# Performance work log

Measured on AMD Instinct MI355X. Metric: run time of the kernel, lower is better.

## Reference

```python
import jax, jax.numpy as jnp
import numpy as np

V, E, H, L = 50257, 256, 1024, 2   # vocab, embed_dim, hidden_dim, num_layers
B, T, K = 64, 80, 5                # batch, max_len, top_k
TEMP = 0.75
TWO_PI_OVER_24 = np.float32(2.0 * np.pi / 24.0)


def setup_inputs() -> dict:
    key = jax.random.key(0)
    ks = jax.random.split(key, 12)
    n = lambda i, shape, s: (jax.random.normal(ks[i], shape, jnp.float32) * s)
    hours = jax.random.uniform(ks[0], (B,), jnp.float32) * 24.0
    return {
        "hours": hours,
        "tp_w1": n(1, (2, H), 0.5),
        "tp_b1": jnp.zeros((H,), jnp.float32),
        "tp_w2": n(2, (H, 2 * L * H), 0.02),
        "tp_b2": jnp.zeros((2 * L * H,), jnp.float32),
        "embed": n(3, (V, E), 0.1).at[0].set(0.0),  # padding_idx=0 row zeroed
        "w_ih0": n(4, (E, 4 * H), 0.05),
        "w_hh0": n(5, (H, 4 * H), 0.05),
        "b0": jnp.zeros((4 * H,), jnp.float32),     # b_ih + b_hh combined
        "w_ih1": n(6, (H, 4 * H), 0.05),
        "w_hh1": n(7, (H, 4 * H), 0.05),
        "b1": jnp.zeros((4 * H,), jnp.float32),
        "fc_w": n(8, (H, V), 0.02),
        "fc_b": jnp.zeros((V,), jnp.float32),
        "sos_id": 1,
    }


def _lstm_cell(x, h, c, w_ih, w_hh, b):
    # torch gate order: i, f, g, o
    g = x @ w_ih + h @ w_hh + b
    i, f, gg, o = jnp.split(g, 4, axis=-1)
    c2 = jax.nn.sigmoid(f) * c + jax.nn.sigmoid(i) * jnp.tanh(gg)
    h2 = jax.nn.sigmoid(o) * jnp.tanh(c2)
    return h2, c2


def reference(hours, tp_w1, tp_b1, tp_w2, tp_b2, embed,
              w_ih0, w_hh0, b0, w_ih1, w_hh1, b1, fc_w, fc_b, sos_id):
    # _encode_time: sin/cos of hour angle -> MLP -> (h0, c0) per layer
    a = hours * TWO_PI_OVER_24
    feat = jnp.stack([jnp.sin(a), jnp.cos(a)], axis=-1)          # [B,2]
    tp = jnp.tanh(feat @ tp_w1 + tp_b1) @ tp_w2 + tp_b2          # [B,2*L*H]
    tp = tp.reshape(B, L, 2, H)
    h = jnp.transpose(tp[:, :, 0, :], (1, 0, 2))                 # [L,B,H]
    c = jnp.transpose(tp[:, :, 1, :], (1, 0, 2))                 # [L,B,H]

    keys = jax.random.split(jax.random.key(42), T)

    def step(carry, k):
        h, c, tok = carry
        x = embed[tok]                                           # [B,E]
        h0n, c0n = _lstm_cell(x, h[0], c[0], w_ih0, w_hh0, b0)
        h1n, c1n = _lstm_cell(h0n, h[1], c[1], w_ih1, w_hh1, b1)
        logits = (h1n @ fc_w + fc_b) / TEMP                      # [B,V]
        topv, topi = jax.lax.top_k(logits, K)                    # [B,K]
        probs = jax.nn.softmax(topv, axis=-1)
        sel = jax.random.categorical(k, topv, axis=-1)           # [B], == multinomial(probs)
        nxt = jnp.take_along_axis(topi, sel[:, None], axis=1)[:, 0]
        return (jnp.stack([h0n, h1n]), jnp.stack([c0n, c1n]), nxt), (nxt, probs)

    tok0 = jnp.full((B,), sos_id, jnp.int32)
    _, (toks, probs) = jax.lax.scan(step, (h, c, tok0), keys)
    # toks: [T,B] -> [B,T]; probs: [T,B,K] -> [B,T,K]
    return jnp.transpose(toks, (1, 0)), jnp.transpose(probs, (1, 0, 2))
```

## Files before the change

### kernel.cpp

```cpp
#include <hip/hip_runtime.h>
#include <math.h>
#include <stdint.h>
#include <limits.h>

#define VSZ 50257
#define ESZ 256
#define HSZ 1024
#define BSZ 64
#define TSZ 80
#define GC  4096
#define NFCB 786
#define NCAND (NFCB*5)
#define NSLOT 13
#define NREF 16

typedef unsigned int u32;
typedef unsigned short u16;
typedef double f64x4 __attribute__((ext_vector_type(4)));
typedef float f32x4v __attribute__((ext_vector_type(4)));
typedef __bf16 bf16x8 __attribute__((ext_vector_type(8)));
union BFrag { u16 u[8]; bf16x8 v; };

__device__ __forceinline__ u16 f2bf(float f) {
  u32 x = __float_as_uint(f);
  return (u16)((x + 0x7FFFu + ((x >> 16) & 1u)) >> 16);
}
__device__ __forceinline__ float bf2f(u16 h) { return __uint_as_float(((u32)h) << 16); }

__device__ __forceinline__ void tf2x32(u32 k0, u32 k1, u32& x0, u32& x1) {
  u32 ks2 = k0 ^ k1 ^ 0x1BD11BDAu;
  x0 += k0; x1 += k1;
#define RND(r) { x0 += x1; x1 = (x1 << r) | (x1 >> (32 - r)); x1 ^= x0; }
  RND(13) RND(15) RND(26) RND(6)
  x0 += k1; x1 += ks2 + 1u;
  RND(17) RND(29) RND(16) RND(24)
  x0 += ks2; x1 += k0 + 2u;
  RND(13) RND(15) RND(26) RND(6)
  x0 += k0; x1 += k1 + 3u;
  RND(17) RND(29) RND(16) RND(24)
  x0 += k1; x1 += ks2 + 4u;
  RND(13) RND(15) RND(26) RND(6)
  x0 += ks2; x1 += k0 + 5u;
#undef RND
}

__device__ __forceinline__ double dsig(double x) { return 0.5 + 0.5 * tanh(0.5 * x); }

__device__ __forceinline__ void ins5(double v, int i, double* tv, int* ti) {
  bool beat4 = (v > tv[4]) || (v == tv[4] && i < ti[4]);
  if (!beat4) return;
  tv[4] = v; ti[4] = i;
#pragma unroll
  for (int p = 4; p > 0; --p) {
    bool sw = (tv[p] > tv[p-1]) || (tv[p] == tv[p-1] && ti[p] < ti[p-1]);
    double a0 = sw ? tv[p] : tv[p-1]; double a1 = sw ? tv[p-1] : tv[p];
    tv[p-1] = a0; tv[p] = a1;
    int b0 = sw ? ti[p] : ti[p-1]; int b1 = sw ? ti[p-1] : ti[p];
    ti[p-1] = b0; ti[p] = b1;
  }
}

__device__ __forceinline__ double dref(int m, int n) {
  int s = 0;
#pragma unroll
  for (int k = 0; k < 4; ++k) s += (4*m + k + 1) * (16*k + n + 1);
  return (double)s;
}

__global__ __launch_bounds__(64) void k_probe(int* __restrict__ fbp) {
  int l = threadIdx.x;
  int lane16 = l & 15, sub = l >> 4;
  {
    double av = (double)(4 * lane16 + sub + 1);
    double bv = (double)(16 * sub + lane16 + 1);
    f64x4 acc = {0., 0., 0., 0.};
    acc = __builtin_amdgcn_mfma_f64_16x16x4f64(av, bv, acc, 0, 0, 0);
    bool o0 = true, o1 = true, o2 = true, o3 = true;
#pragma unroll
    for (int j = 0; j < 4; ++j) {
      double d = acc[j];
      o0 = o0 && (d == dref(4 * sub + j, lane16));
      o1 = o1 && (d == dref(lane16, 4 * sub + j));
      o2 = o2 && (d == dref(sub + 4 * j, lane16));
      o3 = o3 && (d == dref(lane16, sub + 4 * j));
    }
    int a0 = __all(o0), a1 = __all(o1), a2 = __all(o2), a3 = __all(o3);
    if (l == 0) { fbp[0] = a0 ? 0 : a1 ? 1 : a2 ? 2 : 3; fbp[1] = 0; }
  }
  {
    BFrag fa, fbv;
#pragma unroll
    for (int i = 0; i < 8; ++i) {
      int k = sub * 8 + i;
      fa.u[i]  = f2bf((float)((lane16 * 5 + k * 3) % 63 + 1));
      fbv.u[i] = f2bf((float)((k * 7 + lane16 * 11) % 61 + 1));
    }
    f32x4v c = {0.f, 0.f, 0.f, 0.f};
    c = __builtin_amdgcn_mfma_f32_16x16x32_bf16(fa.v, fbv.v, c, 0, 0, 0);
    bool okb = true;
#pragma unroll
    for (int j = 0; j < 4; ++j) {
      int mm = sub * 4 + j, nn = lane16;
      int ref = 0;
      for (int k = 0; k < 32; ++k) ref += ((mm*5 + k*3) % 63 + 1) * ((k*7 + nn*11) % 61 + 1);
      okb = okb && (c[j] == (float)ref);
    }
    int allb = __all(okb);
    if (l == 0) fbp[2] = allb;
  }
}

__global__ __launch_bounds__(256) void k_wconv(const float* __restrict__ W, u16* __restrict__ whT) {
  __shared__ u16 tile[64][65];
  int vb = blockIdx.x * 64, kb = blockIdx.y * 64;
  int tid = threadIdx.x;
#pragma unroll
  for (int i = 0; i < 16; ++i) {
    int r = i * 4 + (tid >> 6), c = tid & 63;
    int v = vb + c;
    tile[c][r] = (v < VSZ) ? f2bf(W[(size_t)(kb + r) * VSZ + v]) : (u16)0;
  }
  __syncthreads();
#pragma unroll
  for (int i = 0; i < 16; ++i) {
    int r = i * 4 + (tid >> 6), c = tid & 63;
    int v = vb + r;
    if (v < VSZ) whT[(size_t)v * 1024 + kb + c] = tile[r][c];
  }
}

__global__ __launch_bounds__(256) void k_rng(double* __restrict__ gum) {
  int idx = blockIdx.x * 256 + threadIdx.x;
  if (idx >= TSZ * 320) return;
  int t = idx / 320, m = idx % 320;
  u32 a0 = 0u, a1 = (u32)t;
  tf2x32(0u, 42u, a0, a1);
  u32 x0 = 0u, x1 = (u32)m;
  tf2x32(a0, a1, x0, x1);
  u32 bits = x0 ^ x1;
  const float TINY = 1.17549435082228750797e-38f;
  float f = __uint_as_float((bits >> 9) | 0x3f800000u) - 1.0f;
  float u = f + TINY;
  u = fmaxf(TINY, u);
  gum[idx] = -log(-log((double)u));
}

__global__ __launch_bounds__(256) void k_time1(const float* __restrict__ hours, const float* __restrict__ w1,
                                               const float* __restrict__ bb1, double* __restrict__ tp1T) {
  int idx = blockIdx.x * 256 + threadIdx.x;
  int b = idx & 63, hcol = idx >> 6;
  const float TPO = (float)(2.0 * 3.14159265358979323846 / 24.0);
  float af = hours[b] * TPO;
  double a = (double)af;
  double sv = sin(a), cv = cos(a);
  double vv = tanh(sv * (double)w1[hcol] + cv * (double)w1[HSZ + hcol] + (double)bb1[hcol]);
  tp1T[(size_t)hcol * 64 + b] = vv;
}

__global__ __launch_bounds__(256) void k_gemm_simple(const double* __restrict__ XTa, const float* __restrict__ Wa,
                                                     int Ka, int Sa, double* __restrict__ part) {
  int j = blockIdx.x * 256 + threadIdx.x;
  if (j >= GC) return;
  int s = blockIdx.y;
  int kc = Ka / Sa, k0 = s * kc;
  double acc[BSZ];
#pragma unroll
  for (int b = 0; b < BSZ; ++b) acc[b] = 0.0;
  const float* wp = Wa + (size_t)k0 * GC + j;
  const double* xp = XTa + (size_t)k0 * 64;
  for (int k = 0; k < kc; ++k) {
    double wv = (double)wp[0]; wp += GC;
#pragma unroll
    for (int b = 0; b < BSZ; ++b) acc[b] = fma(wv, xp[b], acc[b]);
    xp += 64;
  }
  double* o = part + ((size_t)s * 64) * GC + j;
#pragma unroll
  for (int b = 0; b < BSZ; ++b) o[(size_t)b * GC] = acc[b];
}

__global__ __launch_bounds__(256) void k_t2r(const double* __restrict__ part, const float* __restrict__ b2,
                                             double* __restrict__ h0T, double* __restrict__ c0,
                                             double* __restrict__ h1T, double* __restrict__ c1) {
  int b = blockIdx.y;
  int j = blockIdx.x * 256 + threadIdx.x;
  double acc = (double)b2[j];
  for (int s = 0; s < 8; ++s) acc += part[((size_t)s * 64 + b) * GC + j];
  int l = j >> 11, half = (j >> 10) & 1, hcol = j & 1023;
  if (half == 0) (l ? h1T : h0T)[(size_t)hcol * 64 + b] = acc;
  else           (l ? c1 : c0)[(size_t)b * HSZ + hcol] = acc;
}

__global__ __launch_bounds__(256, 4) void k_lstm_mfma(const double* __restrict__ x0, const float* __restrict__ W0,
                                                      const double* __restrict__ x1, const float* __restrict__ W1,
                                                      const double* __restrict__ x2, const float* __restrict__ W2,
                                                      int s1, int s2, double* __restrict__ part,
                                                      const int* __restrict__ fbp) {
  int conv = fbp[0] & 3;
  __shared__ double xs[64 * 64];
  int tid = threadIdx.x;
  int l = tid & 63, wv = tid >> 6;
  int sub = l >> 4, lane16 = l & 15;
  int colbase = blockIdx.x * 64;
  int s = blockIdx.y;
  const double* XT; const float* W; int k0;
  if (s < s1)      { XT = x0; W = W0; k0 = s * 256; }
  else if (s < s2) { XT = x1; W = W1; k0 = (s - s1) * 256; }
  else             { XT = x2; W = W2; k0 = (s - s2) * 256; }
  int colA = colbase + wv * 16 + lane16;
  f64x4 a0 = {0.,0.,0.,0.}, a1 = {0.,0.,0.,0.}, a2 = {0.,0.,0.,0.}, a3 = {0.,0.,0.,0.};
  const float* wp = W + (size_t)(k0 + sub) * GC + colA;
  float ab[8];
#pragma unroll
  for (int u = 0; u < 8; ++u) { ab[u] = wp[0]; wp += (size_t)4 * GC; }
  for (int ch = 0; ch < 4; ++ch) {
    __syncthreads();
    const double2* src = (const double2*)(XT + (size_t)(k0 + ch * 64) * 64);
    double2* dst = (double2*)xs;
    for (int i = tid; i < 2048; i += 256) dst[i] = src[i];
    __syncthreads();
#pragma unroll
    for (int g = 0; g < 2; ++g) {
#pragma unroll
      for (int u = 0; u < 8; ++u) {
        int ks = g * 8 + u;
        int step = ch * 16 + ks;
        float nv = 0.f;
        if (step + 8 < 64) nv = wp[0];
        wp += (size_t)4 * GC;
        double av = (double)ab[u];
        const double* bp = xs + (ks * 4 + sub) * 64 + lane16;
        double b0 = bp[0], b1 = bp[16], b2 = bp[32], b3 = bp[48];
        a0 = __builtin_amdgcn_mfma_f64_16x16x4f64(av, b0, a0, 0, 0, 0);
        a1 = __builtin_amdgcn_mfma_f64_16x16x4f64(av, b1, a1, 0, 0, 0);
        a2 = __builtin_amdgcn_mfma_f64_16x16x4f64(av, b2, a2, 0, 0, 0);
        a3 = __builtin_amdgcn_mfma_f64_16x16x4f64(av, b3, a3, 0, 0, 0);
        ab[u] = nv;
      }
    }
  }
#pragma unroll
  for (int j = 0; j < 4; ++j) {
    int m = (conv == 0) ? sub * 4 + j : (conv == 2) ? sub + 4 * j : lane16;
    int n = (conv == 0) ? lane16 : (conv == 2) ? lane16 : ((conv == 1) ? sub * 4 + j : sub + 4 * j);
    size_t base = ((size_t)s * 64 + n) * GC + colbase + wv * 16 + m;
    part[base]                   = a0[j];
    part[base + (size_t)16 * GC] = a1[j];
    part[base + (size_t)32 * GC] = a2[j];
    part[base + (size_t)48 * GC] = a3[j];
  }
}

__global__ __launch_bounds__(256) void k_cell(const double* __restrict__ part, int sBeg, int S,
                                              const float* __restrict__ bias,
                                              double* __restrict__ c, double* __restrict__ hT,
                                              int emit, u16* __restrict__ xh) {
  int b = blockIdx.y;
  int hcol = blockIdx.x * 256 + threadIdx.x;
  double gi = (double)bias[hcol];
  double gf = (double)bias[1024 + hcol];
  double gg = (double)bias[2048 + hcol];
  double go = (double)bias[3072 + hcol];
#pragma unroll 4
  for (int s = sBeg; s < sBeg + S; ++s) {
    const double* p = part + ((size_t)s * 64 + b) * GC;
    gi += p[hcol]; gf += p[1024 + hcol]; gg += p[2048 + hcol]; go += p[3072 + hcol];
  }
  size_t ci = (size_t)b * HSZ + hcol;
  double cn = dsig(gf) * c[ci] + dsig(gi) * tanh(gg);
  double hn = dsig(go) * tanh(cn);
  c[ci] = cn;
  hT[(size_t)hcol * 64 + b] = hn;
  if (emit)
    xh[(size_t)(hcol >> 7) * 8192 + (size_t)b * 128 + (hcol & 127)] = f2bf((float)hn);
}

__global__ __launch_bounds__(256, 4) void k_fcbf(const u16* __restrict__ xhg, const u16* __restrict__ whT,
                                                 const float* __restrict__ fcb,
                                                 double* __restrict__ candV, int* __restrict__ candI,
                                                 const int* __restrict__ fbp) {
  if (fbp[2] == 0) return;
  __shared__ double xs[64 * 64];
  u16* lx = (u16*)xs;
  int tid = threadIdx.x;
  int l = tid & 63, wv = tid >> 6;
  int sub = l >> 4, lane16 = l & 15;
  int vbase = blockIdx.x * 64;
  int colA = min(vbase + wv * 16 + lane16, VSZ - 1);
  const u16* wrow = whT + (size_t)colA * 1024;
  f32x4v acc0 = {0,0,0,0}, acc1 = {0,0,0,0}, acc2 = {0,0,0,0}, acc3 = {0,0,0,0};
  for (int ch = 0; ch < 8; ++ch) {
    bf16x8 wh0 = *(const bf16x8*)(wrow + ch * 128 + 0 * 32 + sub * 8);
    bf16x8 wh1 = *(const bf16x8*)(wrow + ch * 128 + 1 * 32 + sub * 8);
    bf16x8 wh2 = *(const bf16x8*)(wrow + ch * 128 + 2 * 32 + sub * 8);
    bf16x8 wh3 = *(const bf16x8*)(wrow + ch * 128 + 3 * 32 + sub * 8);
    __syncthreads();
    {
      const uint4* sg = (const uint4*)(xhg + (size_t)ch * 8192);
      uint4* dl = (uint4*)lx;
#pragma unroll
      for (int i = 0; i < 4; ++i) {
        int u = tid + i * 256;
        int bswz = u >> 4, g = u & 15;
        dl[(bswz << 4) | (g ^ (bswz & 7))] = sg[u];
      }
    }
    __syncthreads();
#pragma unroll
    for (int kt = 0; kt < 4; ++kt) {
      bf16x8 whv = (kt == 0) ? wh0 : (kt == 1) ? wh1 : (kt == 2) ? wh2 : wh3;
#define BT_STEP(BT, ACC) {                                                              \
        int bb = BT * 16 + lane16;                                                      \
        const bf16x8* bp2 = (const bf16x8*)lx + ((bb << 4) | ((kt * 4 + sub) ^ (bb & 7))); \
        ACC = __builtin_amdgcn_mfma_f32_16x16x32_bf16(whv, *bp2, ACC, 0, 0, 0); }
      BT_STEP(0, acc0)
      BT_STEP(1, acc1)
      BT_STEP(2, acc2)
      BT_STEP(3, acc3)
#undef BT_STEP
    }
  }
  __syncthreads();
#pragma unroll
  for (int j = 0; j < 4; ++j) {
    int vl = wv * 16 + sub * 4 + j;
    int v = vbase + vl;
    bool okv = (v < VSZ);
    double bi = okv ? (double)fcb[min(v, VSZ - 1)] : 0.0;
    int b0i = lane16, b1i = 16 + lane16, b2i = 32 + lane16, b3i = 48 + lane16;
    xs[b0i * 64 + ((vl + b0i) & 63)] = okv ? ((double)acc0[j] + bi) / 0.75 : -INFINITY;
    xs[b1i * 64 + ((vl + b1i) & 63)] = okv ? ((double)acc1[j] + bi) / 0.75 : -INFINITY;
    xs[b2i * 64 + ((vl + b2i) & 63)] = okv ? ((double)acc2[j] + bi) / 0.75 : -INFINITY;
    xs[b3i * 64 + ((vl + b3i) & 63)] = okv ? ((double)acc3[j] + bi) / 0.75 : -INFINITY;
  }
  __syncthreads();
  if (tid < 64) {
    int b = tid;
    double tv[5]; int ti[5];
#pragma unroll
    for (int p = 0; p < 5; ++p) { tv[p] = -INFINITY; ti[p] = INT_MAX; }
    for (int vl2 = 0; vl2 < 64; ++vl2)
      ins5(xs[b * 64 + ((vl2 + b) & 63)], vbase + vl2, tv, ti);
#pragma unroll
    for (int r = 0; r < 5; ++r) {
      candV[(size_t)b * NCAND + blockIdx.x * 5 + r] = tv[r];
      candI[(size_t)b * NCAND + blockIdx.x * 5 + r] = ti[r];
    }
  }
}

__global__ __launch_bounds__(256, 4) void k_fcf64(const double* __restrict__ h1T, const float* __restrict__ W,
                                                  const float* __restrict__ fcb,
                                                  double* __restrict__ candV, int* __restrict__ candI,
                                                  const int* __restrict__ fbp) {
  int conv = fbp[0] & 3;
  __shared__ double xs[64 * 64];
  int tid = threadIdx.x;
  int l = tid & 63, wv = tid >> 6;
  int sub = l >> 4, lane16 = l & 15;
  int vbase = blockIdx.x * 64;
  int colA = min(vbase + wv * 16 + lane16, VSZ - 1);
  f64x4 a0 = {0.,0.,0.,0.}, a1 = {0.,0.,0.,0.}, a2 = {0.,0.,0.,0.}, a3 = {0.,0.,0.,0.};
  const float* wp = W + (size_t)sub * VSZ + colA;
  float ab[8];
#pragma unroll
  for (int u = 0; u < 8; ++u) { ab[u] = wp[0]; wp += (size_t)4 * VSZ; }
  for (int ch = 0; ch < 16; ++ch) {
    __syncthreads();
    const double2* src = (const double2*)(h1T + (size_t)ch * 64 * 64);
    double2* dst = (double2*)xs;
    for (int i = tid; i < 2048; i += 256) dst[i] = src[i];
    __syncthreads();
#pragma unroll
    for (int g = 0; g < 2; ++g) {
#pragma unroll
      for (int u = 0; u < 8; ++u) {
        int ks = g * 8 + u;
        int step = ch * 16 + ks;
        float nv = 0.f;
        if (step + 8 < 256) nv = wp[0];
        wp += (size_t)4 * VSZ;
        double av = (double)ab[u];
        const double* bp = xs + (ks * 4 + sub) * 64 + lane16;
        double b0 = bp[0], b1 = bp[16], b2 = bp[32], b3 = bp[48];
        a0 = __builtin_amdgcn_mfma_f64_16x16x4f64(av, b0, a0, 0, 0, 0);
        a1 = __builtin_amdgcn_mfma_f64_16x16x4f64(av, b1, a1, 0, 0, 0);
        a2 = __builtin_amdgcn_mfma_f64_16x16x4f64(av, b2, a2, 0, 0, 0);
        a3 = __builtin_amdgcn_mfma_f64_16x16x4f64(av, b3, a3, 0, 0, 0);
        ab[u] = nv;
      }
    }
  }
  __syncthreads();
#pragma unroll
  for (int j = 0; j < 4; ++j) {
    int m = (conv == 0) ? sub * 4 + j : (conv == 2) ? sub + 4 * j : lane16;
    int n = (conv == 0) ? lane16 : (conv == 2) ? lane16 : ((conv == 1) ? sub * 4 + j : sub + 4 * j);
    int vl = wv * 16 + m;
    int v = vbase + vl;
    bool okv = (v < VSZ);
    double bi = okv ? (double)fcb[min(v, VSZ - 1)] : 0.0;
    int b0i = n, b1i = 16 + n, b2i = 32 + n, b3i = 48 + n;
    xs[b0i * 64 + ((vl + b0i) & 63)] = okv ? (a0[j] + bi) / 0.75 : -INFINITY;
    xs[b1i * 64 + ((vl + b1i) & 63)] = okv ? (a1[j] + bi) / 0.75 : -INFINITY;
    xs[b2i * 64 + ((vl + b2i) & 63)] = okv ? (a2[j] + bi) / 0.75 : -INFINITY;
    xs[b3i * 64 + ((vl + b3i) & 63)] = okv ? (a3[j] + bi) / 0.75 : -INFINITY;
  }
  __syncthreads();
  if (tid < 64) {
    int b = tid;
    double tv[5]; int ti[5];
#pragma unroll
    for (int p = 0; p < 5; ++p) { tv[p] = -INFINITY; ti[p] = INT_MAX; }
    for (int vl2 = 0; vl2 < 64; ++vl2)
      ins5(xs[b * 64 + ((vl2 + b) & 63)], vbase + vl2, tv, ti);
#pragma unroll
    for (int r = 0; r < 5; ++r) {
      candV[(size_t)b * NCAND + blockIdx.x * 5 + r] = tv[r];
      candI[(size_t)b * NCAND + blockIdx.x * 5 + r] = ti[r];
    }
  }
}

__global__ __launch_bounds__(256) void k_rfin(const double* __restrict__ candV, const int* __restrict__ candI,
                                              const float* __restrict__ W, const float* __restrict__ fcb,
                                              const double* __restrict__ h1T,
                                              const double* __restrict__ gum, int t,
                                              const float* __restrict__ embed,
                                              float* __restrict__ out, double* __restrict__ xt0) {
  __shared__ float sv[NCAND];
  __shared__ int   si[NCAND];
  __shared__ double exS[NREF];
  __shared__ float wvv[4]; __shared__ int wvi[4]; __shared__ int wvs[4];
  int b = blockIdx.x, tid = threadIdx.x;
  int l = tid & 63, wvd = tid >> 6;
  for (int e = tid; e < NCAND; e += 256) {
    sv[e] = (float)candV[(size_t)b * NCAND + e];
    si[e] = candI[(size_t)b * NCAND + e];
  }
  __syncthreads();
  int cidx[NREF];
#pragma unroll
  for (int r = 0; r < NREF; ++r) {
    float bv = -INFINITY; int bi = INT_MAX, bs = 0;
    for (int e = tid; e < NCAND; e += 256) {
      float v = sv[e]; int i2 = si[e];
      if (v > bv || (v == bv && i2 < bi)) { bv = v; bi = i2; bs = e; }
    }
#pragma unroll
    for (int off = 1; off < 64; off <<= 1) {
      float ov = __shfl_xor(bv, off, 64);
      int oi = __shfl_xor(bi, off, 64);
      int os = __shfl_xor(bs, off, 64);
      if (ov > bv || (ov == bv && oi < bi)) { bv = ov; bi = oi; bs = os; }
    }
    if (l == 0) { wvv[wvd] = bv; wvi[wvd] = bi; wvs[wvd] = bs; }
    __syncthreads();
    float fv = wvv[0]; int fi = wvi[0], fs = wvs[0];
#pragma unroll
    for (int q = 1; q < 4; ++q) {
      float ov = wvv[q]; int oi = wvi[q], os = wvs[q];
      if (ov > fv || (ov == fv && oi < fi)) { fv = ov; fi = oi; fs = os; }
    }
    cidx[r] = fi;
    __syncthreads();
    if (tid == 0) sv[fs] = -INFINITY;
    __syncthreads();
  }
#pragma unroll
  for (int rr = 0; rr < 4; ++rr) {
    int c = wvd + rr * 4;
    int vc = cidx[c];
    double p = 0.0;
#pragma unroll
    for (int i = 0; i < 16; ++i) {
      int k = i * 64 + l;
      p = fma((double)W[(size_t)k * VSZ + vc], h1T[(size_t)k * 64 + b], p);
    }
#pragma unroll
    for (int off = 1; off < 64; off <<= 1) p += __shfl_xor(p, off, 64);
    if (l == 0) exS[c] = (p + (double)fcb[vc]) / 0.75;
  }
  __syncthreads();
  double tv[5]; int ti[5];
#pragma unroll
  for (int p = 0; p < 5; ++p) { tv[p] = -INFINITY; ti[p] = INT_MAX; }
#pragma unroll
  for (int c = 0; c < NREF; ++c) ins5(exS[c], cidx[c], tv, ti);
  const double* g = gum + (size_t)t * 320 + b * 5;
  double bestv = tv[0] + g[0]; int best = 0;
#pragma unroll
  for (int k2 = 1; k2 < 5; ++k2) { double vv2 = tv[k2] + g[k2]; if (vv2 > bestv) { bestv = vv2; best = k2; } }
  int nxt = ti[best];
  if (tid == 0) {
    out[b * TSZ + t] = (float)nxt;
    double m = tv[0];
    double exx[5]; double s = 0.0;
#pragma unroll
    for (int k2 = 0; k2 < 5; ++k2) { exx[k2] = exp(tv[k2] - m); s += exx[k2]; }
    float* po = out + BSZ * TSZ + ((size_t)b * TSZ + t) * 5;
#pragma unroll
    for (int k2 = 0; k2 < 5; ++k2) po[k2] = (float)(exx[k2] / s);
  }
  xt0[(size_t)tid * 64 + b] = (double)embed[(size_t)nxt * ESZ + tid];
}

__global__ __launch_bounds__(256) void k_emb0(const float* __restrict__ embed, const int* __restrict__ sos,
                                              double* __restrict__ xt0) {
  int idx = blockIdx.x * 256 + threadIdx.x;
  int b = idx & 63, k = idx >> 6;
  xt0[(size_t)k * 64 + b] = (double)embed[(size_t)sos[0] * ESZ + k];
}

extern "C" void kernel_launch(void* const* d_in, const int* in_sizes, int n_in,
                              void* d_out, int out_size, void* d_ws, size_t ws_size,
                              hipStream_t stream) {
  const float* hours = (const float*)d_in[0];
  const float* tp_w1 = (const float*)d_in[1];
  const float* tp_b1 = (const float*)d_in[2];
  const float* tp_w2 = (const float*)d_in[3];
  const float* tp_b2 = (const float*)d_in[4];
  const float* embed = (const float*)d_in[5];
  const float* w_ih0 = (const float*)d_in[6];
  const float* w_hh0 = (const float*)d_in[7];
  const float* b0    = (const float*)d_in[8];
  const float* w_ih1 = (const float*)d_in[9];
  const float* w_hh1 = (const float*)d_in[10];
  const float* b1    = (const float*)d_in[11];
  const float* fc_w  = (const float*)d_in[12];
  const float* fc_b  = (const float*)d_in[13];
  const int*   sos   = (const int*)d_in[14];
  float* out = (float*)d_out;

  char* w = (char*)d_ws;
  double* part = (double*)w;  w += (size_t)NSLOT * 64 * GC * 8;
  double* xt0  = (double*)w;  w += (size_t)ESZ * 64 * 8;
  double* h0T  = (double*)w;  w += (size_t)HSZ * 64 * 8;
  double* h1T  = (double*)w;  w += (size_t)HSZ * 64 * 8;
  double* c0   = (double*)w;  w += (size_t)BSZ * HSZ * 8;
  double* c1   = (double*)w;  w += (size_t)BSZ * HSZ * 8;
  double* tp1T = (double*)w;  w += (size_t)HSZ * 64 * 8;
  double* gum  = (double*)w;  w += (size_t)TSZ * 320 * 8;
  double* candV = (double*)w; w += (size_t)BSZ * NCAND * 8;
  int*    candI = (int*)w;    w += (size_t)BSZ * NCAND * 4;
  int*    fbuf  = (int*)w;    w += 64;
  u16*    xhg   = (u16*)w;    w += (size_t)HSZ * 64 * 2;
  u16*    whT   = (u16*)w;    w += (size_t)VSZ * 1024 * 2;
  size_t need = (size_t)(w - (char*)d_ws);
  int useBF = (ws_size >= need) ? 1 : 0;

  k_probe<<<dim3(1), dim3(64), 0, stream>>>(fbuf);
  k_rng<<<dim3(100), dim3(256), 0, stream>>>(gum);
  k_time1<<<dim3(256), dim3(256), 0, stream>>>(hours, tp_w1, tp_b1, tp1T);
  k_gemm_simple<<<dim3(16, 8), dim3(256), 0, stream>>>(tp1T, tp_w2, 1024, 8, part);
  k_t2r<<<dim3(16, 64), dim3(256), 0, stream>>>(part, tp_b2, h0T, c0, h1T, c1);
  k_emb0<<<dim3(64), dim3(256), 0, stream>>>(embed, sos, xt0);
  if (useBF)
    k_wconv<<<dim3(786, 16), dim3(256), 0, stream>>>(fc_w, whT);

  double* part9 = part + (size_t)9 * 64 * GC;
  for (int t = 0; t < TSZ; ++t) {
    k_lstm_mfma<<<dim3(64, 9), dim3(256), 0, stream>>>(xt0, w_ih0, h0T, w_hh0, h1T, w_hh1, 1, 5, part, fbuf);
    k_cell<<<dim3(4, 64), dim3(256), 0, stream>>>(part, 0, 5, b0, c0, h0T, 0, xhg);
    k_lstm_mfma<<<dim3(64, 4), dim3(256), 0, stream>>>(h0T, w_ih1, h0T, w_ih1, h0T, w_ih1, 4, 4, part9, fbuf);
    k_cell<<<dim3(4, 64), dim3(256), 0, stream>>>(part, 5, 8, b1, c1, h1T, 1, xhg);
    if (useBF)
      k_fcbf<<<dim3(NFCB), dim3(256), 0, stream>>>(xhg, whT, fc_b, candV, candI, fbuf);
    else
      k_fcf64<<<dim3(NFCB), dim3(256), 0, stream>>>(h1T, fc_w, fc_b, candV, candI, fbuf);
    k_rfin<<<dim3(64), dim3(256), 0, stream>>>(candV, candI, fc_w, fc_b, h1T, gum, t, embed, out, xt0);
  }
}
```

Before: 18.98 ms.

## Fuse per-timestep decode kernels into one persistent cooperative megakernel

```diff
diff --git a/kernel.cpp b/kernel.cpp
--- a/kernel.cpp
+++ b/kernel.cpp
@@ -1,4 +1,5 @@
 #include <hip/hip_runtime.h>
+#include <hip/hip_cooperative_groups.h>
 #include <math.h>
 #include <stdint.h>
 #include <limits.h>
@@ -13,6 +14,9 @@
 #define NCAND (NFCB*5)
 #define NSLOT 13
 #define NREF 16
+#define MGRID 576
+
+namespace cg = cooperative_groups;
 
 typedef unsigned int u32;
 typedef unsigned short u16;
@@ -191,22 +195,12 @@
   else           (l ? c1 : c0)[(size_t)b * HSZ + hcol] = acc;
 }
 
-__global__ __launch_bounds__(256, 4) void k_lstm_mfma(const double* __restrict__ x0, const float* __restrict__ W0,
-                                                      const double* __restrict__ x1, const float* __restrict__ W1,
-                                                      const double* __restrict__ x2, const float* __restrict__ W2,
-                                                      int s1, int s2, double* __restrict__ part,
-                                                      const int* __restrict__ fbp) {
-  int conv = fbp[0] & 3;
-  __shared__ double xs[64 * 64];
-  int tid = threadIdx.x;
+
+__device__ __forceinline__ void lstm_unit(int cb, int slot, const double* XT, const float* W, int k0,
+                                          double* part, int conv, double* xs, int tid) {
   int l = tid & 63, wv = tid >> 6;
   int sub = l >> 4, lane16 = l & 15;
-  int colbase = blockIdx.x * 64;
-  int s = blockIdx.y;
-  const double* XT; const float* W; int k0;
-  if (s < s1)      { XT = x0; W = W0; k0 = s * 256; }
-  else if (s < s2) { XT = x1; W = W1; k0 = (s - s1) * 256; }
-  else             { XT = x2; W = W2; k0 = (s - s2) * 256; }
+  int colbase = cb * 64;
   int colA = colbase + wv * 16 + lane16;
   f64x4 a0 = {0.,0.,0.,0.}, a1 = {0.,0.,0.,0.}, a2 = {0.,0.,0.,0.}, a3 = {0.,0.,0.,0.};
   const float* wp = W + (size_t)(k0 + sub) * GC + colA;
@@ -239,11 +233,12 @@
       }
     }
   }
+  __syncthreads();
 #pragma unroll
   for (int j = 0; j < 4; ++j) {
     int m = (conv == 0) ? sub * 4 + j : (conv == 2) ? sub + 4 * j : lane16;
     int n = (conv == 0) ? lane16 : (conv == 2) ? lane16 : ((conv == 1) ? sub * 4 + j : sub + 4 * j);
-    size_t base = ((size_t)s * 64 + n) * GC + colbase + wv * 16 + m;
+    size_t base = ((size_t)slot * 64 + n) * GC + colbase + wv * 16 + m;
     part[base]                   = a0[j];
     part[base + (size_t)16 * GC] = a1[j];
     part[base + (size_t)32 * GC] = a2[j];
@@ -251,12 +246,11 @@
   }
 }
 
-__global__ __launch_bounds__(256) void k_cell(const double* __restrict__ part, int sBeg, int S,
-                                              const float* __restrict__ bias,
-                                              double* __restrict__ c, double* __restrict__ hT,
-                                              int emit, u16* __restrict__ xh) {
-  int b = blockIdx.y;
-  int hcol = blockIdx.x * 256 + threadIdx.x;
+__device__ __forceinline__ void cell_unit(int u, const double* part, int sBeg, int S,
+                                          const float* bias, double* c, double* hT,
+                                          int emit, u16* xh, int tid) {
+  int b = u & 63;
+  int hcol = (u >> 6) * 256 + tid;
   double gi = (double)bias[hcol];
   double gf = (double)bias[1024 + hcol];
   double gg = (double)bias[2048 + hcol];
@@ -275,17 +269,12 @@
     xh[(size_t)(hcol >> 7) * 8192 + (size_t)b * 128 + (hcol & 127)] = f2bf((float)hn);
 }
 
-__global__ __launch_bounds__(256, 4) void k_fcbf(const u16* __restrict__ xhg, const u16* __restrict__ whT,
-                                                 const float* __restrict__ fcb,
-                                                 double* __restrict__ candV, int* __restrict__ candI,
-                                                 const int* __restrict__ fbp) {
-  if (fbp[2] == 0) return;
-  __shared__ double xs[64 * 64];
+__device__ __forceinline__ void fcbf_unit(int u, const u16* xhg, const u16* whT, const float* fcb,
+                                          double* candV, int* candI, double* xs, int tid) {
   u16* lx = (u16*)xs;
-  int tid = threadIdx.x;
   int l = tid & 63, wv = tid >> 6;
   int sub = l >> 4, lane16 = l & 15;
-  int vbase = blockIdx.x * 64;
+  int vbase = u * 64;
   int colA = min(vbase + wv * 16 + lane16, VSZ - 1);
   const u16* wrow = whT + (size_t)colA * 1024;
   f32x4v acc0 = {0,0,0,0}, acc1 = {0,0,0,0}, acc2 = {0,0,0,0}, acc3 = {0,0,0,0};
@@ -300,9 +289,9 @@
       uint4* dl = (uint4*)lx;
 #pragma unroll
       for (int i = 0; i < 4; ++i) {
-        int u = tid + i * 256;
-        int bswz = u >> 4, g = u & 15;
-        dl[(bswz << 4) | (g ^ (bswz & 7))] = sg[u];
+        int uu = tid + i * 256;
+        int bswz = uu >> 4, g = uu & 15;
+        dl[(bswz << 4) | (g ^ (bswz & 7))] = sg[uu];
       }
     }
     __syncthreads();
@@ -343,28 +332,24 @@
       ins5(xs[b * 64 + ((vl2 + b) & 63)], vbase + vl2, tv, ti);
 #pragma unroll
     for (int r = 0; r < 5; ++r) {
-      candV[(size_t)b * NCAND + blockIdx.x * 5 + r] = tv[r];
-      candI[(size_t)b * NCAND + blockIdx.x * 5 + r] = ti[r];
-    }
-  }
-}
-
-__global__ __launch_bounds__(256, 4) void k_fcf64(const double* __restrict__ h1T, const float* __restrict__ W,
-                                                  const float* __restrict__ fcb,
-                                                  double* __restrict__ candV, int* __restrict__ candI,
-                                                  const int* __restrict__ fbp) {
-  int conv = fbp[0] & 3;
-  __shared__ double xs[64 * 64];
-  int tid = threadIdx.x;
+      candV[(size_t)b * NCAND + u * 5 + r] = tv[r];
+      candI[(size_t)b * NCAND + u * 5 + r] = ti[r];
+    }
+  }
+  __syncthreads();
+}
+
+__device__ __forceinline__ void fcf64_unit(int u, const double* h1T, const float* W, const float* fcb,
+                                           double* candV, int* candI, int conv, double* xs, int tid) {
   int l = tid & 63, wv = tid >> 6;
   int sub = l >> 4, lane16 = l & 15;
-  int vbase = blockIdx.x * 64;
+  int vbase = u * 64;
   int colA = min(vbase + wv * 16 + lane16, VSZ - 1);
   f64x4 a0 = {0.,0.,0.,0.}, a1 = {0.,0.,0.,0.}, a2 = {0.,0.,0.,0.}, a3 = {0.,0.,0.,0.};
   const float* wp = W + (size_t)sub * VSZ + colA;
   float ab[8];
 #pragma unroll
-  for (int u = 0; u < 8; ++u) { ab[u] = wp[0]; wp += (size_t)4 * VSZ; }
+  for (int uu = 0; uu < 8; ++uu) { ab[uu] = wp[0]; wp += (size_t)4 * VSZ; }
   for (int ch = 0; ch < 16; ++ch) {
     __syncthreads();
     const double2* src = (const double2*)(h1T + (size_t)ch * 64 * 64);
@@ -374,20 +359,20 @@
 #pragma unroll
     for (int g = 0; g < 2; ++g) {
 #pragma unroll
-      for (int u = 0; u < 8; ++u) {
-        int ks = g * 8 + u;
+      for (int uu = 0; uu < 8; ++uu) {
+        int ks = g * 8 + uu;
         int step = ch * 16 + ks;
         float nv = 0.f;
         if (step + 8 < 256) nv = wp[0];
         wp += (size_t)4 * VSZ;
-        double av = (double)ab[u];
+        double av = (double)ab[uu];
         const double* bp = xs + (ks * 4 + sub) * 64 + lane16;
         double b0 = bp[0], b1 = bp[16], b2 = bp[32], b3 = bp[48];
         a0 = __builtin_amdgcn_mfma_f64_16x16x4f64(av, b0, a0, 0, 0, 0);
         a1 = __builtin_amdgcn_mfma_f64_16x16x4f64(av, b1, a1, 0, 0, 0);
         a2 = __builtin_amdgcn_mfma_f64_16x16x4f64(av, b2, a2, 0, 0, 0);
         a3 = __builtin_amdgcn_mfma_f64_16x16x4f64(av, b3, a3, 0, 0, 0);
-        ab[u] = nv;
+        ab[uu] = nv;
       }
     }
   }
@@ -416,10 +401,184 @@
       ins5(xs[b * 64 + ((vl2 + b) & 63)], vbase + vl2, tv, ti);
 #pragma unroll
     for (int r = 0; r < 5; ++r) {
-      candV[(size_t)b * NCAND + blockIdx.x * 5 + r] = tv[r];
-      candI[(size_t)b * NCAND + blockIdx.x * 5 + r] = ti[r];
-    }
-  }
+      candV[(size_t)b * NCAND + u * 5 + r] = tv[r];
+      candI[(size_t)b * NCAND + u * 5 + r] = ti[r];
+    }
+  }
+  __syncthreads();
+}
+
+__device__ __forceinline__ void rfin_unit(int b, const double* candV, const int* candI,
+                                          const float* W, const float* fcb, const double* h1T,
+                                          const double* gum, int t, const float* embed,
+                                          float* out, double* xt0, char* smem,
+                                          double* exS, float* wvv, int* wvi, int* wvs, int tid) {
+  float* sv = (float*)smem;
+  int*   si = (int*)(smem + NCAND * 4);
+  int l = tid & 63, wvd = tid >> 6;
+  for (int e = tid; e < NCAND; e += 256) {
+    sv[e] = (float)candV[(size_t)b * NCAND + e];
+    si[e] = candI[(size_t)b * NCAND + e];
+  }
+  __syncthreads();
+  int cidx[NREF];
+#pragma unroll
+  for (int r = 0; r < NREF; ++r) {
+    float bv = -INFINITY; int bi = INT_MAX, bs = 0;
+    for (int e = tid; e < NCAND; e += 256) {
+      float v = sv[e]; int i2 = si[e];
+      if (v > bv || (v == bv && i2 < bi)) { bv = v; bi = i2; bs = e; }
+    }
+#pragma unroll
+    for (int off = 1; off < 64; off <<= 1) {
+      float ov = __shfl_xor(bv, off, 64);
+      int oi = __shfl_xor(bi, off, 64);
+      int os = __shfl_xor(bs, off, 64);
+      if (ov > bv || (ov == bv && oi < bi)) { bv = ov; bi = oi; bs = os; }
+    }
+    if (l == 0) { wvv[wvd] = bv; wvi[wvd] = bi; wvs[wvd] = bs; }
+    __syncthreads();
+    float fv = wvv[0]; int fi = wvi[0], fs = wvs[0];
+#pragma unroll
+    for (int q = 1; q < 4; ++q) {
+      float ov = wvv[q]; int oi = wvi[q], os = wvs[q];
+      if (ov > fv || (ov == fv && oi < fi)) { fv = ov; fi = oi; fs = os; }
+    }
+    cidx[r] = fi;
+    __syncthreads();
+    if (tid == 0) sv[fs] = -INFINITY;
+    __syncthreads();
+  }
+#pragma unroll
+  for (int rr = 0; rr < 4; ++rr) {
+    int c = wvd + rr * 4;
+    int vc = cidx[c];
+    double p = 0.0;
+#pragma unroll
+    for (int i = 0; i < 16; ++i) {
+      int k = i * 64 + l;
+      p = fma((double)W[(size_t)k * VSZ + vc], h1T[(size_t)k * 64 + b], p);
+    }
+#pragma unroll
+    for (int off = 1; off < 64; off <<= 1) p += __shfl_xor(p, off, 64);
+    if (l == 0) exS[c] = (p + (double)fcb[vc]) / 0.75;
+  }
+  __syncthreads();
+  double tv[5]; int ti[5];
+#pragma unroll
+  for (int p = 0; p < 5; ++p) { tv[p] = -INFINITY; ti[p] = INT_MAX; }
+#pragma unroll
+  for (int c = 0; c < NREF; ++c) ins5(exS[c], cidx[c], tv, ti);
+  const double* g = gum + (size_t)t * 320 + b * 5;
+  double bestv = tv[0] + g[0]; int best = 0;
+#pragma unroll
+  for (int k2 = 1; k2 < 5; ++k2) { double vv2 = tv[k2] + g[k2]; if (vv2 > bestv) { bestv = vv2; best = k2; } }
+  int nxt = ti[best];
+  if (tid == 0) {
+    out[b * TSZ + t] = (float)nxt;
+    double m = tv[0];
+    double exx[5]; double s = 0.0;
+#pragma unroll
+    for (int k2 = 0; k2 < 5; ++k2) { exx[k2] = exp(tv[k2] - m); s += exx[k2]; }
+    float* po = out + BSZ * TSZ + ((size_t)b * TSZ + t) * 5;
+#pragma unroll
+    for (int k2 = 0; k2 < 5; ++k2) po[k2] = (float)(exx[k2] / s);
+  }
+  xt0[(size_t)tid * 64 + b] = (double)embed[(size_t)nxt * ESZ + tid];
+  __syncthreads();
+}
+
+struct MArgs {
+  double *xt0, *h0T, *h1T, *c0, *c1, *part, *gum, *candV;
+  int *candI, *fbuf;
+  u16 *xhg, *whT;
+  const float *w_ih0, *w_hh0, *b0, *w_ih1, *w_hh1, *b1, *fc_w, *fc_b, *embed;
+  float *out;
+  int useBF;
+};
+
+__global__ __launch_bounds__(256, 3) void k_mega(MArgs A) {
+  cg::grid_group grid = cg::this_grid();
+  __shared__ alignas(16) char smem[32768];
+  __shared__ double exS[NREF];
+  __shared__ float wvv[4]; __shared__ int wvi[4]; __shared__ int wvs[4];
+  double* xs = (double*)smem;
+  int tid = threadIdx.x;
+  int conv = A.fbuf[0] & 3;
+  int bf = A.useBF && (A.fbuf[2] != 0);
+  double* part9 = A.part + (size_t)9 * 64 * GC;
+  for (int t = 0; t < TSZ; ++t) {
+    for (int u = blockIdx.x; u < 576; u += gridDim.x) {
+      int cb = u & 63, s = u >> 6;
+      const double* XT; const float* W; int k0;
+      if (s < 1)      { XT = A.xt0; W = A.w_ih0; k0 = 0; }
+      else if (s < 5) { XT = A.h0T; W = A.w_hh0; k0 = (s - 1) * 256; }
+      else            { XT = A.h1T; W = A.w_hh1; k0 = (s - 5) * 256; }
+      lstm_unit(cb, s, XT, W, k0, A.part, conv, xs, tid);
+    }
+    grid.sync();
+    for (int u = blockIdx.x; u < 256; u += gridDim.x)
+      cell_unit(u, A.part, 0, 5, A.b0, A.c0, A.h0T, 0, A.xhg, tid);
+    grid.sync();
+    for (int u = blockIdx.x; u < 256; u += gridDim.x) {
+      int cb = u & 63, s = u >> 6;
+      lstm_unit(cb, 9 + s, A.h0T, A.w_ih1, s * 256, A.part, conv, xs, tid);
+    }
+    grid.sync();
+    for (int u = blockIdx.x; u < 256; u += gridDim.x)
+      cell_unit(u, A.part, 5, 8, A.b1, A.c1, A.h1T, 1, A.xhg, tid);
+    grid.sync();
+    if (bf) {
+      for (int u = blockIdx.x; u < NFCB; u += gridDim.x)
+        fcbf_unit(u, A.xhg, A.whT, A.fc_b, A.candV, A.candI, xs, tid);
+    } else {
+      for (int u = blockIdx.x; u < NFCB; u += gridDim.x)
+        fcf64_unit(u, A.h1T, A.fc_w, A.fc_b, A.candV, A.candI, conv, xs, tid);
+    }
+    grid.sync();
+    for (int u = blockIdx.x; u < 64; u += gridDim.x)
+      rfin_unit(u, A.candV, A.candI, A.fc_w, A.fc_b, A.h1T, A.gum, t, A.embed,
+                A.out, A.xt0, smem, exS, wvv, wvi, wvs, tid);
+    grid.sync();
+  }
+}
+
+
+__global__ __launch_bounds__(256, 4) void k_lstm_mfma(const double* __restrict__ x0, const float* __restrict__ W0,
+                                                      const double* __restrict__ x1, const float* __restrict__ W1,
+                                                      const double* __restrict__ x2, const float* __restrict__ W2,
+                                                      int s1, int s2, double* __restrict__ part,
+                                                      const int* __restrict__ fbp) {
+  __shared__ double xs[64 * 64];
+  int s = blockIdx.y;
+  const double* XT; const float* W; int k0;
+  if (s < s1)      { XT = x0; W = W0; k0 = s * 256; }
+  else if (s < s2) { XT = x1; W = W1; k0 = (s - s1) * 256; }
+  else             { XT = x2; W = W2; k0 = (s - s2) * 256; }
+  lstm_unit(blockIdx.x, s, XT, W, k0, part, fbp[0] & 3, xs, threadIdx.x);
+}
+
+__global__ __launch_bounds__(256) void k_cell(const double* __restrict__ part, int sBeg, int S,
+                                              const float* __restrict__ bias,
+                                              double* __restrict__ c, double* __restrict__ hT,
+                                              int emit, u16* __restrict__ xh) {
+  cell_unit(blockIdx.x * 64 + blockIdx.y, part, sBeg, S, bias, c, hT, emit, xh, threadIdx.x);
+}
+
+__global__ __launch_bounds__(256, 4) void k_fcbf(const u16* __restrict__ xhg, const u16* __restrict__ whT,
+                                                 const float* __restrict__ fcb,
+                                                 double* __restrict__ candV, int* __restrict__ candI,
+                                                 const int* __restrict__ fbp) {
+  __shared__ double xs[64 * 64];
+  fcbf_unit(blockIdx.x, xhg, whT, fcb, candV, candI, xs, threadIdx.x);
+}
+
+__global__ __launch_bounds__(256, 4) void k_fcf64(const double* __restrict__ h1T, const float* __restrict__ W,
+                                                  const float* __restrict__ fcb,
+                                                  double* __restrict__ candV, int* __restrict__ candI,
+                                                  const int* __restrict__ fbp) {
+  __shared__ double xs[64 * 64];
+  fcf64_unit(blockIdx.x, h1T, W, fcb, candV, candI, fbp[0] & 3, xs, threadIdx.x);
 }
 
 __global__ __launch_bounds__(256) void k_rfin(const double* __restrict__ candV, const int* __restrict__ candI,
@@ -428,81 +587,11 @@
                                               const double* __restrict__ gum, int t,
                                               const float* __restrict__ embed,
                                               float* __restrict__ out, double* __restrict__ xt0) {
-  __shared__ float sv[NCAND];
-  __shared__ int   si[NCAND];
+  __shared__ alignas(16) char smem[32768];
   __shared__ double exS[NREF];
   __shared__ float wvv[4]; __shared__ int wvi[4]; __shared__ int wvs[4];
-  int b = blockIdx.x, tid = threadIdx.x;
-  int l = tid & 63, wvd = tid >> 6;
-  for (int e = tid; e < NCAND; e += 256) {
-    sv[e] = (float)candV[(size_t)b * NCAND + e];
-    si[e] = candI[(size_t)b * NCAND + e];
-  }
-  __syncthreads();
-  int cidx[NREF];
-#pragma unroll
-  for (int r = 0; r < NREF; ++r) {
-    float bv = -INFINITY; int bi = INT_MAX, bs = 0;
-    for (int e = tid; e < NCAND; e += 256) {
-      float v = sv[e]; int i2 = si[e];
-      if (v > bv || (v == bv && i2 < bi)) { bv = v; bi = i2; bs = e; }
-    }
-#pragma unroll
-    for (int off = 1; off < 64; off <<= 1) {
-      float ov = __shfl_xor(bv, off, 64);
-      int oi = __shfl_xor(bi, off, 64);
-      int os = __shfl_xor(bs, off, 64);
-      if (ov > bv || (ov == bv && oi < bi)) { bv = ov; bi = oi; bs = os; }
-    }
-    if (l == 0) { wvv[wvd] = bv; wvi[wvd] = bi; wvs[wvd] = bs; }
-    __syncthreads();
-    float fv = wvv[0]; int fi = wvi[0], fs = wvs[0];
-#pragma unroll
-    for (int q = 1; q < 4; ++q) {
-      float ov = wvv[q]; int oi = wvi[q], os = wvs[q];
-      if (ov > fv || (ov == fv && oi < fi)) { fv = ov; fi = oi; fs = os; }
-    }
-    cidx[r] = fi;
-    __syncthreads();
-    if (tid == 0) sv[fs] = -INFINITY;
-    __syncthreads();
-  }
-#pragma unroll
-  for (int rr = 0; rr < 4; ++rr) {
-    int c = wvd + rr * 4;
-    int vc = cidx[c];
-    double p = 0.0;
-#pragma unroll
-    for (int i = 0; i < 16; ++i) {
-      int k = i * 64 + l;
-      p = fma((double)W[(size_t)k * VSZ + vc], h1T[(size_t)k * 64 + b], p);
-    }
-#pragma unroll
-    for (int off = 1; off < 64; off <<= 1) p += __shfl_xor(p, off, 64);
-    if (l == 0) exS[c] = (p + (double)fcb[vc]) / 0.75;
-  }
-  __syncthreads();
-  double tv[5]; int ti[5];
-#pragma unroll
-  for (int p = 0; p < 5; ++p) { tv[p] = -INFINITY; ti[p] = INT_MAX; }
-#pragma unroll
-  for (int c = 0; c < NREF; ++c) ins5(exS[c], cidx[c], tv, ti);
-  const double* g = gum + (size_t)t * 320 + b * 5;
-  double bestv = tv[0] + g[0]; int best = 0;
-#pragma unroll
-  for (int k2 = 1; k2 < 5; ++k2) { double vv2 = tv[k2] + g[k2]; if (vv2 > bestv) { bestv = vv2; best = k2; } }
-  int nxt = ti[best];
-  if (tid == 0) {
-    out[b * TSZ + t] = (float)nxt;
-    double m = tv[0];
-    double exx[5]; double s = 0.0;
-#pragma unroll
-    for (int k2 = 0; k2 < 5; ++k2) { exx[k2] = exp(tv[k2] - m); s += exx[k2]; }
-    float* po = out + BSZ * TSZ + ((size_t)b * TSZ + t) * 5;
-#pragma unroll
-    for (int k2 = 0; k2 < 5; ++k2) po[k2] = (float)(exx[k2] / s);
-  }
-  xt0[(size_t)tid * 64 + b] = (double)embed[(size_t)nxt * ESZ + tid];
+  rfin_unit(blockIdx.x, candV, candI, W, fcb, h1T, gum, t, embed, out, xt0,
+            smem, exS, wvv, wvi, wvs, threadIdx.x);
 }
 
 __global__ __launch_bounds__(256) void k_emb0(const float* __restrict__ embed, const int* __restrict__ sos,
@@ -558,16 +647,25 @@
   if (useBF)
     k_wconv<<<dim3(786, 16), dim3(256), 0, stream>>>(fc_w, whT);
 
-  double* part9 = part + (size_t)9 * 64 * GC;
-  for (int t = 0; t < TSZ; ++t) {
-    k_lstm_mfma<<<dim3(64, 9), dim3(256), 0, stream>>>(xt0, w_ih0, h0T, w_hh0, h1T, w_hh1, 1, 5, part, fbuf);
-    k_cell<<<dim3(4, 64), dim3(256), 0, stream>>>(part, 0, 5, b0, c0, h0T, 0, xhg);
-    k_lstm_mfma<<<dim3(64, 4), dim3(256), 0, stream>>>(h0T, w_ih1, h0T, w_ih1, h0T, w_ih1, 4, 4, part9, fbuf);
-    k_cell<<<dim3(4, 64), dim3(256), 0, stream>>>(part, 5, 8, b1, c1, h1T, 1, xhg);
-    if (useBF)
-      k_fcbf<<<dim3(NFCB), dim3(256), 0, stream>>>(xhg, whT, fc_b, candV, candI, fbuf);
-    else
-      k_fcf64<<<dim3(NFCB), dim3(256), 0, stream>>>(h1T, fc_w, fc_b, candV, candI, fbuf);
-    k_rfin<<<dim3(64), dim3(256), 0, stream>>>(candV, candI, fc_w, fc_b, h1T, gum, t, embed, out, xt0);
-  }
-}
+  MArgs A;
+  A.xt0 = xt0; A.h0T = h0T; A.h1T = h1T; A.c0 = c0; A.c1 = c1; A.part = part;
+  A.gum = gum; A.candV = candV; A.candI = candI; A.fbuf = fbuf; A.xhg = xhg; A.whT = whT;
+  A.w_ih0 = w_ih0; A.w_hh0 = w_hh0; A.b0 = b0; A.w_ih1 = w_ih1; A.w_hh1 = w_hh1; A.b1 = b1;
+  A.fc_w = fc_w; A.fc_b = fc_b; A.embed = embed; A.out = out; A.useBF = useBF;
+  void* kargs[] = { (void*)&A };
+  hipError_t ce = hipLaunchCooperativeKernel((void*)k_mega, dim3(MGRID), dim3(256), kargs, 0, stream);
+  if (ce != hipSuccess) {
+    double* part9 = part + (size_t)9 * 64 * GC;
+    for (int t = 0; t < TSZ; ++t) {
+      k_lstm_mfma<<<dim3(64, 9), dim3(256), 0, stream>>>(xt0, w_ih0, h0T, w_hh0, h1T, w_hh1, 1, 5, part, fbuf);
+      k_cell<<<dim3(4, 64), dim3(256), 0, stream>>>(part, 0, 5, b0, c0, h0T, 0, xhg);
+      k_lstm_mfma<<<dim3(64, 4), dim3(256), 0, stream>>>(h0T, w_ih1, h0T, w_ih1, h0T, w_ih1, 4, 4, part9, fbuf);
+      k_cell<<<dim3(4, 64), dim3(256), 0, stream>>>(part, 5, 8, b1, c1, h1T, 1, xhg);
+      if (useBF)
+        k_fcbf<<<dim3(NFCB), dim3(256), 0, stream>>>(xhg, whT, fc_b, candV, candI, fbuf);
+      else
+        k_fcf64<<<dim3(NFCB), dim3(256), 0, stream>>>(h1T, fc_w, fc_b, candV, candI, fbuf);
+      k_rfin<<<dim3(64), dim3(256), 0, stream>>>(candV, candI, fc_w, fc_b, h1T, gum, t, embed, out, xt0);
+    }
+  }
+}
```

Result: slower. 63.70 ms (+235.6%).
